# Optimization experiments

Hardware: AMD Instinct MI355X
Metric: run time of the kernel (lower is better)

Reference implementation:

```python
import jax, jax.numpy as jnp
import numpy as np

DIM = 1024
HID = 2048
OUT = 1024
NE = 8
TOPK = 2

def _xavier(key, shape):
    fan_in, fan_out = shape[-2], shape[-1]
    lim = jnp.sqrt(6.0 / (fan_in + fan_out))
    return jax.random.uniform(key, shape, jnp.float32, -lim, lim)

def setup_inputs() -> dict:
    key = jax.random.key(0)
    ks = jax.random.split(key, 8)
    X = jax.random.normal(ks[0], (4, 1024, DIM), jnp.float32)
    # stacked expert params: [NE, ...]
    W1 = _xavier(ks[1], (NE, DIM, HID))
    W3 = _xavier(ks[2], (NE, DIM, HID))
    W2 = _xavier(ks[3], (NE, HID, OUT))
    b1 = jnp.zeros((NE, HID), jnp.float32)
    b3 = jnp.zeros((NE, HID), jnp.float32)
    b2 = jnp.zeros((NE, OUT), jnp.float32)
    Wg = _xavier(ks[4], (DIM, NE))
    bg = jnp.zeros((NE,), jnp.float32)
    Wf = _xavier(ks[5], (OUT, OUT))
    bf = jnp.zeros((OUT,), jnp.float32)
    return {"X": X, "W1": W1, "b1": b1, "W3": W3, "b3": b3, "W2": W2, "b2": b2,
            "Wg": Wg, "bg": bg, "Wf": Wf, "bf": bf}

def reference(X, W1, b1, W3, b3, W2, b2, Wg, bg, Wf, bf):
    # gating: [B,S,E]
    gating = jax.nn.softmax(X @ Wg + bg, axis=-1)
    # top-k via argsort (matches original: ascending sort, take last k)
    top_k_indices = jnp.argsort(gating, axis=-1)[..., -TOPK:]  # [B,S,K]
    # dense all-expert SwiGLU FFN: [B,S,E,O]
    h1 = jnp.einsum('bsd,edh->bseh', X, W1) + b1  # [B,S,E,H]
    h3 = jnp.einsum('bsd,edh->bseh', X, W3) + b3
    h = jax.nn.silu(h1 * h3)
    expert_outputs = jnp.einsum('bseh,eho->bseo', h, W2) + b2  # [B,S,E,O]
    # gather top-k expert outputs
    topk_out = jnp.take_along_axis(expert_outputs, top_k_indices[..., None], axis=2)  # [B,S,K,O]
    topk_w = jnp.take_along_axis(gating, top_k_indices, axis=-1)  # [B,S,K]
    mixed = jnp.sum(topk_w[..., None] * topk_out, axis=2)  # [B,S,O]
    return mixed @ Wf + bf
```

## Files before the change

kernel.cpp:

```cpp
#include <hip/hip_runtime.h>

#define DIM  1024
#define HID  2048
#define OUTD 1024
#define NE   8
#define NTOK 4096

using bf16x8 = __attribute__((ext_vector_type(8))) short;
using f32x4  = __attribute__((ext_vector_type(4))) float;

__device__ __forceinline__ unsigned short f2bf(float f) {
  unsigned int u = __builtin_bit_cast(unsigned int, f);
  u += 0x7fff + ((u >> 16) & 1);
  return (unsigned short)(u >> 16);
}
__device__ __forceinline__ float b2f(unsigned short u) {
  unsigned int v = (unsigned int)u << 16;
  return __builtin_bit_cast(float, v);
}

__device__ __forceinline__ void gload16(const void* g, void* l) {
  __builtin_amdgcn_global_load_lds(
      (const __attribute__((address_space(1))) void*)g,
      (__attribute__((address_space(3))) void*)l, 16, 0, 0);
}

__device__ __forceinline__ void tc_tile(const float* __restrict__ inp, int C,
                                        unsigned short* __restrict__ op, int R,
                                        int c0, int r0, float (*tile)[33],
                                        int interleave, int s) {
  int tx = threadIdx.x & 31, ty = threadIdx.x >> 5;
#pragma unroll
  for (int j = 0; j < 4; j++)
    tile[ty + j * 8][tx] = inp[(size_t)(r0 + ty + j * 8) * C + c0 + tx];
  __syncthreads();
  int c = threadIdx.x >> 3, q = threadIdx.x & 7;
  int h = c0 + c;
  int orow = interleave ? (32 * (h >> 4) + 16 * s + (h & 15)) : h;
  ushort4 u;
  u.x = f2bf(tile[q * 4 + 0][c]); u.y = f2bf(tile[q * 4 + 1][c]);
  u.z = f2bf(tile[q * 4 + 2][c]); u.w = f2bf(tile[q * 4 + 3][c]);
  *(ushort4*)&op[(size_t)orow * R + r0 + q * 4] = u;
}

__global__ void tcast_i_kernel(const float* __restrict__ W1,
                               const float* __restrict__ W3,
                               unsigned short* __restrict__ out) {
  __shared__ float tile[32][33];
  int z = blockIdx.z, e = z & 7, s = z >> 3;
  const float* inp = (s ? W3 : W1) + (size_t)e * DIM * HID;
  unsigned short* op = out + (size_t)e * 2 * HID * DIM;
  tc_tile(inp, HID, op, DIM, blockIdx.x * 32, blockIdx.y * 32, tile, 1, s);
}

__global__ void tcast2_kernel(const float* __restrict__ W2, const float* __restrict__ Wf,
                              unsigned short* __restrict__ W2t,
                              unsigned short* __restrict__ Wft) {
  __shared__ float tile[32][33];
  int z = blockIdx.z;
  if (z < NE) {
    tc_tile(W2 + (size_t)z * HID * OUTD, OUTD, W2t + (size_t)z * OUTD * HID, HID,
            blockIdx.x * 32, blockIdx.y * 32, tile, 0, 0);
  } else {
    if (blockIdx.y >= DIM / 32) return;
    tc_tile(Wf, OUTD, Wft, DIM, blockIdx.x * 32, blockIdx.y * 32, tile, 0, 0);
  }
}

__global__ __launch_bounds__(256) void gating_kernel(
    const float* __restrict__ X, const float* __restrict__ Wg,
    const float* __restrict__ bg, unsigned short* __restrict__ Xb,
    int* __restrict__ topk_pack, float* __restrict__ topk_w,
    int* __restrict__ blkcnt) {
  __shared__ float wgs[NE][DIM];
  __shared__ int hist[NE];
  const int tid = threadIdx.x;
  for (int d = tid; d < DIM; d += 256) {
#pragma unroll
    for (int e = 0; e < NE; e++) wgs[e][d] = Wg[d * NE + e];
  }
  if (tid < NE) hist[tid] = 0;
  __syncthreads();
  const int wave = tid >> 6, lane = tid & 63;
  for (int tk = wave; tk < 32; tk += 4) {
    const int t = blockIdx.x * 32 + tk;
    const float* xr = X + (size_t)t * DIM;
    {
      const float4* xp = (const float4*)(xr + lane * 16);
      float4 v0 = xp[0], v1 = xp[1], v2 = xp[2], v3 = xp[3];
      uint4 w0, w1;
      w0.x = f2bf(v0.x) | ((unsigned)f2bf(v0.y) << 16);
      w0.y = f2bf(v0.z) | ((unsigned)f2bf(v0.w) << 16);
      w0.z = f2bf(v1.x) | ((unsigned)f2bf(v1.y) << 16);
      w0.w = f2bf(v1.z) | ((unsigned)f2bf(v1.w) << 16);
      w1.x = f2bf(v2.x) | ((unsigned)f2bf(v2.y) << 16);
      w1.y = f2bf(v2.z) | ((unsigned)f2bf(v2.w) << 16);
      w1.z = f2bf(v3.x) | ((unsigned)f2bf(v3.y) << 16);
      w1.w = f2bf(v3.z) | ((unsigned)f2bf(v3.w) << 16);
      uint4* op2 = (uint4*)(Xb + (size_t)t * DIM + lane * 16);
      op2[0] = w0; op2[1] = w1;
    }
    float acc[NE];
#pragma unroll
    for (int e = 0; e < NE; e++) acc[e] = 0.f;
#pragma unroll
    for (int j = 0; j < 16; j++) {
      float xv = xr[lane + j * 64];
#pragma unroll
      for (int e = 0; e < NE; e++) acc[e] += xv * wgs[e][lane + j * 64];
    }
#pragma unroll
    for (int e = 0; e < NE; e++) {
#pragma unroll
      for (int off = 32; off > 0; off >>= 1) acc[e] += __shfl_xor(acc[e], off, 64);
    }
    if (lane == 0) {
      float p[NE];
      float mx = -1e30f;
#pragma unroll
      for (int e = 0; e < NE; e++) { p[e] = acc[e] + bg[e]; mx = fmaxf(mx, p[e]); }
      float sum = 0.f;
#pragma unroll
      for (int e = 0; e < NE; e++) { p[e] = expf(p[e] - mx); sum += p[e]; }
      float inv = 1.f / sum;
#pragma unroll
      for (int e = 0; e < NE; e++) p[e] *= inv;
      int i1 = 0; float v1 = p[0];
#pragma unroll
      for (int e = 1; e < NE; e++) if (p[e] >= v1) { v1 = p[e]; i1 = e; }
      int i2 = (i1 == 0) ? 1 : 0; float v2 = p[i2];
#pragma unroll
      for (int e = 0; e < NE; e++) {
        if (e == i1) continue;
        if (p[e] >= v2 && e != i2) { v2 = p[e]; i2 = e; }
      }
      topk_pack[t] = i1 | (i2 << 4);
      topk_w[t * 2 + 0] = v1; topk_w[t * 2 + 1] = v2;
      atomicAdd(&hist[i1], 1); atomicAdd(&hist[i2], 1);
    }
  }
  __syncthreads();
  if (tid < NE) blkcnt[blockIdx.x * NE + tid] = hist[tid];
}

__global__ void scatter_kernel(const int* __restrict__ blkcnt,
                               const int* __restrict__ topk_pack,
                               int* __restrict__ counts, int* __restrict__ row_start,
                               int* __restrict__ tp, int* __restrict__ list) {
  __shared__ int lofs[NE];
  const int lane = threadIdx.x;
  const int myb = blockIdx.x;
  int s = 0, t = 0;
#pragma unroll
  for (int e = 0; e < NE; e++) {
    int c0 = blkcnt[lane * NE + e], c1 = blkcnt[(lane + 64) * NE + e];
    int tote = c0 + c1;
    int pre = (lane < myb ? c0 : 0) + (lane + 64 < myb ? c1 : 0);
#pragma unroll
    for (int off = 32; off > 0; off >>= 1) {
      tote += __shfl_xor(tote, off, 64);
      pre  += __shfl_xor(pre,  off, 64);
    }
    if (lane == 0) lofs[e] = s + pre;
    if (myb == 0 && lane == 0) { counts[e] = tote; row_start[e] = s; tp[e] = t; }
    s += tote; t += (tote + 127) >> 7;
  }
  if (myb == 0 && lane == 0) tp[NE] = t;
  __syncthreads();
  if (lane < 32) {
    int tok = myb * 32 + lane;
    int pk = topk_pack[tok];
    int e1 = pk & 15, e2 = (pk >> 4) & 15;
    int p1 = atomicAdd(&lofs[e1], 1); list[p1] = tok << 1;
    int p2 = atomicAdd(&lofs[e2], 1); list[p2] = (tok << 1) | 1;
  }
}

__global__ __launch_bounds__(512, 4) void ffn_a_kernel(
    const unsigned short* __restrict__ Xb,
    const unsigned short* __restrict__ W13t,
    const float* __restrict__ b1, const float* __restrict__ b3,
    const int* __restrict__ counts, const int* __restrict__ row_start,
    const int* __restrict__ tp, const int* __restrict__ list,
    unsigned short* __restrict__ h_buf) {
  __shared__ unsigned short S[24576];
  const int by = blockIdx.y;
  if (by >= tp[NE]) return;
  int e = 0;
#pragma unroll
  for (int k = 1; k < NE; k++) if (by >= tp[k]) e = k;
  const int ne = counts[e], rs = row_start[e];
  const int m0 = (by - tp[e]) * 128;
  const int n0 = blockIdx.x * 256;

  const int tid = threadIdx.x;
  const int wave = tid >> 6, lane = tid & 63;
  const int lr = lane & 15, lk = lane >> 4;
  const int wm = (wave & 1) * 64, wn = (wave >> 1) * 64;

  const int scs = ((lane & 7) ^ (lane >> 3)) * 8;
  const unsigned short* asrc[2];
  const unsigned short* bsrc[4];
#pragma unroll
  for (int i = 0; i < 2; i++) {
    int sr = i * 64 + wave * 8 + (lane >> 3);
    int rr = m0 + sr; if (rr >= ne) rr = m0;
    int tok = list[rs + rr] >> 1;
    asrc[i] = Xb + (size_t)tok * DIM + scs;
  }
#pragma unroll
  for (int c = 0; c < 4; c++) {
    int sr = c * 64 + wave * 8 + (lane >> 3);
    bsrc[c] = W13t + ((size_t)e * 2 * HID + n0 + sr) * DIM + scs;
  }

  f32x4 acc[4][4];
  const f32x4 zero = {0.f, 0.f, 0.f, 0.f};
#pragma unroll
  for (int m = 0; m < 4; m++)
#pragma unroll
    for (int n = 0; n < 4; n++) acc[m][n] = zero;

  const int sx = lr & 7;

  for (int k0 = 0; k0 < DIM; k0 += 64) {
#pragma unroll
    for (int i = 0; i < 2; i++)
      gload16(asrc[i] + k0, &S[(i * 64 + wave * 8) * 64]);
#pragma unroll
    for (int c = 0; c < 4; c++)
      gload16(bsrc[c] + k0, &S[8192 + (c * 64 + wave * 8) * 64]);
    __syncthreads();
#pragma unroll
    for (int kk = 0; kk < 2; kk++) {
      const int sl = ((kk * 4 + lk) ^ sx) * 8;
      bf16x8 a[4], b[4];
#pragma unroll
      for (int m = 0; m < 4; m++)
        a[m] = *(const bf16x8*)&S[(wm + m * 16 + lr) * 64 + sl];
#pragma unroll
      for (int n = 0; n < 4; n++)
        b[n] = *(const bf16x8*)&S[8192 + (wn + n * 16 + lr) * 64 + sl];
#pragma unroll
      for (int m = 0; m < 4; m++)
#pragma unroll
        for (int n = 0; n < 4; n++)
          acc[m][n] = __builtin_amdgcn_mfma_f32_16x16x32_bf16(a[m], b[n], acc[m][n], 0, 0, 0);
    }
    __syncthreads();
  }

  const int hq = (n0 + wn) >> 5;
#pragma unroll
  for (int g = 0; g < 2; g++) {
    int h = (hq + g) * 16 + lr;
    float b1v = b1[e * HID + h];
    float b3v = b3[e * HID + h];
#pragma unroll
    for (int m = 0; m < 4; m++) {
#pragma unroll
      for (int j = 0; j < 4; j++) {
        int rr = m0 + wm + m * 16 + lk * 4 + j;
        if (rr < ne) {
          float h1 = acc[m][2 * g][j] + b1v;
          float h3 = acc[m][2 * g + 1][j] + b3v;
          float v = h1 * h3;
          h_buf[(size_t)(rs + rr) * HID + h] = f2bf(v / (1.f + expf(-v)));
        }
      }
    }
  }
}

__global__ __launch_bounds__(256, 3) void ffn_b_kernel(
    const unsigned short* __restrict__ h_buf,
    const unsigned short* __restrict__ W2t,
    const float* __restrict__ b2,
    const int* __restrict__ counts, const int* __restrict__ row_start,
    const int* __restrict__ tp, const int* __restrict__ list,
    const float* __restrict__ topk_w, unsigned short* __restrict__ ob) {
  __shared__ unsigned short As[128 * 64];
  __shared__ unsigned short Bs[128 * 64];
  const int by = blockIdx.y;
  if (by >= tp[NE]) return;
  int e = 0;
#pragma unroll
  for (int k = 1; k < NE; k++) if (by >= tp[k]) e = k;
  const int ne = counts[e], rs = row_start[e];
  const int m0 = (by - tp[e]) * 128;
  const int n0 = blockIdx.x * 128;

  const int tid = threadIdx.x;
  const int wave = tid >> 6, lane = tid & 63;
  const int lr = lane & 15, lk = lane >> 4;
  const int wm = (wave >> 1) * 64, wn = (wave & 1) * 64;

  const int scs = ((lane & 7) ^ (lane >> 3)) * 8;
  const unsigned short* asrc[4];
  const unsigned short* bsrc[4];
#pragma unroll
  for (int i = 0; i < 4; i++) {
    int sr = (wave * 4 + i) * 8 + (lane >> 3);
    asrc[i] = h_buf + (size_t)(rs + m0 + sr) * HID + scs;
    bsrc[i] = W2t + ((size_t)e * OUTD + n0 + sr) * HID + scs;
  }

  f32x4 acc[4][4];
  const f32x4 zero = {0.f, 0.f, 0.f, 0.f};
#pragma unroll
  for (int m = 0; m < 4; m++)
#pragma unroll
    for (int n = 0; n < 4; n++) acc[m][n] = zero;

  const int sx = lr & 7;

  for (int k0 = 0; k0 < HID; k0 += 64) {
#pragma unroll
    for (int i = 0; i < 4; i++) {
      gload16(asrc[i] + k0, &As[(wave * 4 + i) * 512]);
      gload16(bsrc[i] + k0, &Bs[(wave * 4 + i) * 512]);
    }
    __syncthreads();
#pragma unroll
    for (int kk = 0; kk < 2; kk++) {
      const int sl = ((kk * 4 + lk) ^ sx) * 8;
      bf16x8 a[4], b[4];
#pragma unroll
      for (int m = 0; m < 4; m++)
        a[m] = *(const bf16x8*)&As[(wm + m * 16 + lr) * 64 + sl];
#pragma unroll
      for (int n = 0; n < 4; n++)
        b[n] = *(const bf16x8*)&Bs[(wn + n * 16 + lr) * 64 + sl];
#pragma unroll
      for (int m = 0; m < 4; m++)
#pragma unroll
        for (int n = 0; n < 4; n++)
          acc[m][n] = __builtin_amdgcn_mfma_f32_16x16x32_bf16(a[m], b[n], acc[m][n], 0, 0, 0);
    }
    __syncthreads();
  }

#pragma unroll
  for (int n = 0; n < 4; n++) {
    int col = n0 + wn + n * 16 + lr;
    float b2v = b2[e * OUTD + col];
#pragma unroll
    for (int m = 0; m < 4; m++) {
#pragma unroll
      for (int j = 0; j < 4; j++) {
        int rr = m0 + wm + m * 16 + lk * 4 + j;
        if (rr < ne) {
          int entry = list[rs + rr];
          float w = topk_w[entry];
          ob[(size_t)entry * OUTD + col] = f2bf(w * (acc[m][n][j] + b2v));
        }
      }
    }
  }
}

__global__ __launch_bounds__(256) void final_kernel(
    const unsigned short* __restrict__ ob, const unsigned short* __restrict__ Wft,
    const float* __restrict__ bfv, float* __restrict__ out) {
  const int bid = blockIdx.x;
  const int n0 = (bid >> 5) * 128;
  const int m0 = ((bid & 7) + 8 * ((bid >> 3) & 3)) * 128;

  __shared__ unsigned short As[128 * 64];
  __shared__ unsigned short Bs[128 * 64];

  const int tid = threadIdx.x;
  const int wave = tid >> 6, lane = tid & 63;
  const int lrow = lane >> 3;
  const int lcol = (lane & 7) * 8;

  const unsigned short* bsrc[4];
#pragma unroll
  for (int i = 0; i < 4; i++) {
    int sr = (wave * 4 + i) * 8 + lrow;
    bsrc[i] = Wft + (size_t)(n0 + sr) * DIM + lcol;
  }

  const int wm = (wave >> 1) * 64, wn = (wave & 1) * 64;
  const int lr = lane & 15, lk = lane >> 4;

  f32x4 acc[4][4];
  const f32x4 zero = {0.f, 0.f, 0.f, 0.f};
#pragma unroll
  for (int m = 0; m < 4; m++)
#pragma unroll
    for (int n = 0; n < 4; n++) acc[m][n] = zero;

  for (int k0 = 0; k0 < DIM; k0 += 64) {
#pragma unroll
    for (int g = 0; g < 8; g++) {
      int idx = g * 256 + tid;
      int r = idx >> 4;
      int c4 = (idx & 15) * 4;
      ushort4 a0 = *(const ushort4*)&ob[((size_t)(m0 + r) * 2) * OUTD + k0 + c4];
      ushort4 a1 = *(const ushort4*)&ob[((size_t)(m0 + r) * 2 + 1) * OUTD + k0 + c4];
      ushort4 u;
      u.x = f2bf(b2f(a0.x) + b2f(a1.x)); u.y = f2bf(b2f(a0.y) + b2f(a1.y));
      u.z = f2bf(b2f(a0.z) + b2f(a1.z)); u.w = f2bf(b2f(a0.w) + b2f(a1.w));
      *(ushort4*)&As[r * 64 + c4] = u;
    }
#pragma unroll
    for (int i = 0; i < 4; i++) gload16(bsrc[i] + k0, &Bs[(wave * 4 + i) * 512]);
    __syncthreads();
#pragma unroll
    for (int kk = 0; kk < 2; kk++) {
      bf16x8 a[4], b[4];
#pragma unroll
      for (int m = 0; m < 4; m++)
        a[m] = *(const bf16x8*)&As[(wm + m * 16 + lr) * 64 + kk * 32 + lk * 8];
#pragma unroll
      for (int n = 0; n < 4; n++)
        b[n] = *(const bf16x8*)&Bs[(wn + n * 16 + lr) * 64 + kk * 32 + lk * 8];
#pragma unroll
      for (int m = 0; m < 4; m++)
#pragma unroll
        for (int n = 0; n < 4; n++)
          acc[m][n] = __builtin_amdgcn_mfma_f32_16x16x32_bf16(a[m], b[n], acc[m][n], 0, 0, 0);
    }
    __syncthreads();
  }

#pragma unroll
  for (int n = 0; n < 4; n++) {
    int col = n0 + wn + n * 16 + lr;
    float bv = bfv[col];
#pragma unroll
    for (int m = 0; m < 4; m++) {
#pragma unroll
      for (int j = 0; j < 4; j++) {
        int r = m0 + wm + m * 16 + lk * 4 + j;
        out[(size_t)r * OUTD + col] = acc[m][n][j] + bv;
      }
    }
  }
}

extern "C" void kernel_launch(void* const* d_in, const int* in_sizes, int n_in,
                              void* d_out, int out_size, void* d_ws, size_t ws_size,
                              hipStream_t stream) {
  const float* X   = (const float*)d_in[0];
  const float* W1  = (const float*)d_in[1];
  const float* b1  = (const float*)d_in[2];
  const float* W3  = (const float*)d_in[3];
  const float* b3  = (const float*)d_in[4];
  const float* W2  = (const float*)d_in[5];
  const float* b2  = (const float*)d_in[6];
  const float* Wg  = (const float*)d_in[7];
  const float* bg  = (const float*)d_in[8];
  const float* Wf  = (const float*)d_in[9];
  const float* bfv = (const float*)d_in[10];
  float* out = (float*)d_out;

  char* p = (char*)d_ws;
  auto alloc = [&](size_t bytes) { char* r = p; p += (bytes + 255) & ~(size_t)255; return r; };
  unsigned short* Xb   = (unsigned short*)alloc((size_t)NTOK * DIM * 2);
  unsigned short* W13t = (unsigned short*)alloc((size_t)NE * 2 * HID * DIM * 2);
  unsigned short* W2t  = (unsigned short*)alloc((size_t)NE * OUTD * HID * 2);
  unsigned short* Wft  = (unsigned short*)alloc((size_t)OUTD * DIM * 2);
  unsigned short* hbuf = (unsigned short*)alloc((size_t)(NTOK * 2 + 256) * HID * 2);
  unsigned short* ob   = (unsigned short*)alloc((size_t)NTOK * 2 * OUTD * 2);
  int* topk_pack       = (int*)alloc(NTOK * 4);
  float* topk_w        = (float*)alloc(NTOK * 2 * 4);
  int* counts          = (int*)alloc(NE * 4);
  int* row_start       = (int*)alloc(NE * 4);
  int* tp              = (int*)alloc((NE + 1) * 4);
  int* blkcnt          = (int*)alloc(128 * NE * 4);
  int* list            = (int*)alloc(NTOK * 2 * 4);

  gating_kernel<<<128, 256, 0, stream>>>(X, Wg, bg, Xb, topk_pack, topk_w, blkcnt);
  tcast_i_kernel<<<dim3(HID / 32, DIM / 32, 16), 256, 0, stream>>>(W1, W3, W13t);
  tcast2_kernel<<<dim3(OUTD / 32, HID / 32, NE + 1), 256, 0, stream>>>(W2, Wf, W2t, Wft);

  scatter_kernel<<<128, 64, 0, stream>>>(blkcnt, topk_pack, counts, row_start, tp, list);

  ffn_a_kernel<<<dim3(2 * HID / 256, 72), 512, 0, stream>>>(
      Xb, W13t, b1, b3, counts, row_start, tp, list, hbuf);
  ffn_b_kernel<<<dim3(OUTD / 128, 72), 256, 0, stream>>>(
      hbuf, W2t, b2, counts, row_start, tp, list, topk_w, ob);
  final_kernel<<<256, 256, 0, stream>>>(ob, Wft, bfv, out);
}
```

Baseline: 315.8 us.

## Shrink GEMM K-tile to 32 with 128x128 blocks and merge weight-cast kernels

The two weight transpose/cast kernels become one flat-grid launch, removing a kernel boundary. Both expert GEMM kernels now use 256-thread blocks with 128x128 output tiles and a 32-wide K step, using half the LDS per block and a new swizzle, with launch bounds raised to 6 blocks per CU. The aim is higher occupancy so more blocks can hide latency. In exchange there are twice as many barriers per unit of K, and ffn_a has half the tile width, so operand reuse per block is lower.

```diff
diff --git a/kernel.cpp b/kernel.cpp
--- a/kernel.cpp
+++ b/kernel.cpp
@@ -43,27 +43,27 @@
   *(ushort4*)&op[(size_t)orow * R + r0 + q * 4] = u;
 }
 
-__global__ void tcast_i_kernel(const float* __restrict__ W1,
-                               const float* __restrict__ W3,
-                               unsigned short* __restrict__ out) {
+__global__ void tcast_all_kernel(const float* __restrict__ W1, const float* __restrict__ W3,
+                                 const float* __restrict__ W2, const float* __restrict__ Wf,
+                                 unsigned short* __restrict__ W13t,
+                                 unsigned short* __restrict__ W2t,
+                                 unsigned short* __restrict__ Wft) {
   __shared__ float tile[32][33];
-  int z = blockIdx.z, e = z & 7, s = z >> 3;
-  const float* inp = (s ? W3 : W1) + (size_t)e * DIM * HID;
-  unsigned short* op = out + (size_t)e * 2 * HID * DIM;
-  tc_tile(inp, HID, op, DIM, blockIdx.x * 32, blockIdx.y * 32, tile, 1, s);
-}
-
-__global__ void tcast2_kernel(const float* __restrict__ W2, const float* __restrict__ Wf,
-                              unsigned short* __restrict__ W2t,
-                              unsigned short* __restrict__ Wft) {
-  __shared__ float tile[32][33];
-  int z = blockIdx.z;
-  if (z < NE) {
+  int b = blockIdx.x;
+  if (b < 32768) {
+    int z = b >> 11, rem = b & 2047;
+    int e = z & 7, s = z >> 3;
+    tc_tile((s ? W3 : W1) + (size_t)e * DIM * HID, HID,
+            W13t + (size_t)e * 2 * HID * DIM, DIM,
+            (rem & 63) * 32, (rem >> 6) * 32, tile, 1, s);
+  } else if (b < 49152) {
+    int i = b - 32768;
+    int z = i >> 11, rem = i & 2047;
     tc_tile(W2 + (size_t)z * HID * OUTD, OUTD, W2t + (size_t)z * OUTD * HID, HID,
-            blockIdx.x * 32, blockIdx.y * 32, tile, 0, 0);
+            (rem & 31) * 32, (rem >> 5) * 32, tile, 0, 0);
   } else {
-    if (blockIdx.y >= DIM / 32) return;
-    tc_tile(Wf, OUTD, Wft, DIM, blockIdx.x * 32, blockIdx.y * 32, tile, 0, 0);
+    int i = b - 49152;
+    tc_tile(Wf, OUTD, Wft, DIM, (i & 31) * 32, (i >> 5) * 32, tile, 0, 0);
   }
 }
 
@@ -176,14 +176,15 @@
   }
 }
 
-__global__ __launch_bounds__(512, 4) void ffn_a_kernel(
+__global__ __launch_bounds__(256, 6) void ffn_a_kernel(
     const unsigned short* __restrict__ Xb,
     const unsigned short* __restrict__ W13t,
     const float* __restrict__ b1, const float* __restrict__ b3,
     const int* __restrict__ counts, const int* __restrict__ row_start,
     const int* __restrict__ tp, const int* __restrict__ list,
     unsigned short* __restrict__ h_buf) {
-  __shared__ unsigned short S[24576];
+  __shared__ unsigned short As[128 * 32];
+  __shared__ unsigned short Bs[128 * 32];
   const int by = blockIdx.y;
   if (by >= tp[NE]) return;
   int e = 0;
@@ -191,27 +192,23 @@
   for (int k = 1; k < NE; k++) if (by >= tp[k]) e = k;
   const int ne = counts[e], rs = row_start[e];
   const int m0 = (by - tp[e]) * 128;
-  const int n0 = blockIdx.x * 256;
+  const int n0 = blockIdx.x * 128;
 
   const int tid = threadIdx.x;
   const int wave = tid >> 6, lane = tid & 63;
   const int lr = lane & 15, lk = lane >> 4;
-  const int wm = (wave & 1) * 64, wn = (wave >> 1) * 64;
-
-  const int scs = ((lane & 7) ^ (lane >> 3)) * 8;
+  const int wm = (wave >> 1) * 64, wn = (wave & 1) * 64;
+
+  const int scs = ((lane & 3) ^ ((lane >> 3) & 3)) * 8;
   const unsigned short* asrc[2];
-  const unsigned short* bsrc[4];
+  const unsigned short* bsrc[2];
 #pragma unroll
   for (int i = 0; i < 2; i++) {
-    int sr = i * 64 + wave * 8 + (lane >> 3);
+    int sr = (wave * 2 + i) * 16 + (lane >> 2);
     int rr = m0 + sr; if (rr >= ne) rr = m0;
     int tok = list[rs + rr] >> 1;
     asrc[i] = Xb + (size_t)tok * DIM + scs;
-  }
-#pragma unroll
-  for (int c = 0; c < 4; c++) {
-    int sr = c * 64 + wave * 8 + (lane >> 3);
-    bsrc[c] = W13t + ((size_t)e * 2 * HID + n0 + sr) * DIM + scs;
+    bsrc[i] = W13t + ((size_t)e * 2 * HID + n0 + sr) * DIM + scs;
   }
 
   f32x4 acc[4][4];
@@ -221,32 +218,27 @@
 #pragma unroll
     for (int n = 0; n < 4; n++) acc[m][n] = zero;
 
-  const int sx = lr & 7;
-
-  for (int k0 = 0; k0 < DIM; k0 += 64) {
-#pragma unroll
-    for (int i = 0; i < 2; i++)
-      gload16(asrc[i] + k0, &S[(i * 64 + wave * 8) * 64]);
-#pragma unroll
-    for (int c = 0; c < 4; c++)
-      gload16(bsrc[c] + k0, &S[8192 + (c * 64 + wave * 8) * 64]);
-    __syncthreads();
-#pragma unroll
-    for (int kk = 0; kk < 2; kk++) {
-      const int sl = ((kk * 4 + lk) ^ sx) * 8;
-      bf16x8 a[4], b[4];
-#pragma unroll
-      for (int m = 0; m < 4; m++)
-        a[m] = *(const bf16x8*)&S[(wm + m * 16 + lr) * 64 + sl];
+  const int sl = (lk ^ ((lr >> 1) & 3)) * 8;
+
+  for (int k0 = 0; k0 < DIM; k0 += 32) {
+#pragma unroll
+    for (int i = 0; i < 2; i++) {
+      gload16(asrc[i] + k0, &As[(wave * 2 + i) * 512]);
+      gload16(bsrc[i] + k0, &Bs[(wave * 2 + i) * 512]);
+    }
+    __syncthreads();
+    bf16x8 a[4], b[4];
+#pragma unroll
+    for (int m = 0; m < 4; m++)
+      a[m] = *(const bf16x8*)&As[(wm + m * 16 + lr) * 32 + sl];
+#pragma unroll
+    for (int n = 0; n < 4; n++)
+      b[n] = *(const bf16x8*)&Bs[(wn + n * 16 + lr) * 32 + sl];
+#pragma unroll
+    for (int m = 0; m < 4; m++)
 #pragma unroll
       for (int n = 0; n < 4; n++)
-        b[n] = *(const bf16x8*)&S[8192 + (wn + n * 16 + lr) * 64 + sl];
-#pragma unroll
-      for (int m = 0; m < 4; m++)
-#pragma unroll
-        for (int n = 0; n < 4; n++)
-          acc[m][n] = __builtin_amdgcn_mfma_f32_16x16x32_bf16(a[m], b[n], acc[m][n], 0, 0, 0);
-    }
+        acc[m][n] = __builtin_amdgcn_mfma_f32_16x16x32_bf16(a[m], b[n], acc[m][n], 0, 0, 0);
     __syncthreads();
   }
 
@@ -272,15 +264,15 @@
   }
 }
 
-__global__ __launch_bounds__(256, 3) void ffn_b_kernel(
+__global__ __launch_bounds__(256, 6) void ffn_b_kernel(
     const unsigned short* __restrict__ h_buf,
     const unsigned short* __restrict__ W2t,
     const float* __restrict__ b2,
     const int* __restrict__ counts, const int* __restrict__ row_start,
     const int* __restrict__ tp, const int* __restrict__ list,
     const float* __restrict__ topk_w, unsigned short* __restrict__ ob) {
-  __shared__ unsigned short As[128 * 64];
-  __shared__ unsigned short Bs[128 * 64];
+  __shared__ unsigned short As[128 * 32];
+  __shared__ unsigned short Bs[128 * 32];
   const int by = blockIdx.y;
   if (by >= tp[NE]) return;
   int e = 0;
@@ -295,12 +287,12 @@
   const int lr = lane & 15, lk = lane >> 4;
   const int wm = (wave >> 1) * 64, wn = (wave & 1) * 64;
 
-  const int scs = ((lane & 7) ^ (lane >> 3)) * 8;
-  const unsigned short* asrc[4];
-  const unsigned short* bsrc[4];
-#pragma unroll
-  for (int i = 0; i < 4; i++) {
-    int sr = (wave * 4 + i) * 8 + (lane >> 3);
+  const int scs = ((lane & 3) ^ ((lane >> 3) & 3)) * 8;
+  const unsigned short* asrc[2];
+  const unsigned short* bsrc[2];
+#pragma unroll
+  for (int i = 0; i < 2; i++) {
+    int sr = (wave * 2 + i) * 16 + (lane >> 2);
     asrc[i] = h_buf + (size_t)(rs + m0 + sr) * HID + scs;
     bsrc[i] = W2t + ((size_t)e * OUTD + n0 + sr) * HID + scs;
   }
@@ -312,31 +304,27 @@
 #pragma unroll
     for (int n = 0; n < 4; n++) acc[m][n] = zero;
 
-  const int sx = lr & 7;
-
-  for (int k0 = 0; k0 < HID; k0 += 64) {
-#pragma unroll
-    for (int i = 0; i < 4; i++) {
-      gload16(asrc[i] + k0, &As[(wave * 4 + i) * 512]);
-      gload16(bsrc[i] + k0, &Bs[(wave * 4 + i) * 512]);
-    }
-    __syncthreads();
-#pragma unroll
-    for (int kk = 0; kk < 2; kk++) {
-      const int sl = ((kk * 4 + lk) ^ sx) * 8;
-      bf16x8 a[4], b[4];
-#pragma unroll
-      for (int m = 0; m < 4; m++)
-        a[m] = *(const bf16x8*)&As[(wm + m * 16 + lr) * 64 + sl];
+  const int sl = (lk ^ ((lr >> 1) & 3)) * 8;
+
+  for (int k0 = 0; k0 < HID; k0 += 32) {
+#pragma unroll
+    for (int i = 0; i < 2; i++) {
+      gload16(asrc[i] + k0, &As[(wave * 2 + i) * 512]);
+      gload16(bsrc[i] + k0, &Bs[(wave * 2 + i) * 512]);
+    }
+    __syncthreads();
+    bf16x8 a[4], b[4];
+#pragma unroll
+    for (int m = 0; m < 4; m++)
+      a[m] = *(const bf16x8*)&As[(wm + m * 16 + lr) * 32 + sl];
+#pragma unroll
+    for (int n = 0; n < 4; n++)
+      b[n] = *(const bf16x8*)&Bs[(wn + n * 16 + lr) * 32 + sl];
+#pragma unroll
+    for (int m = 0; m < 4; m++)
 #pragma unroll
       for (int n = 0; n < 4; n++)
-        b[n] = *(const bf16x8*)&Bs[(wn + n * 16 + lr) * 64 + sl];
-#pragma unroll
-      for (int m = 0; m < 4; m++)
-#pragma unroll
-        for (int n = 0; n < 4; n++)
-          acc[m][n] = __builtin_amdgcn_mfma_f32_16x16x32_bf16(a[m], b[n], acc[m][n], 0, 0, 0);
-    }
+        acc[m][n] = __builtin_amdgcn_mfma_f32_16x16x32_bf16(a[m], b[n], acc[m][n], 0, 0, 0);
     __syncthreads();
   }
 
@@ -473,12 +461,11 @@
   int* list            = (int*)alloc(NTOK * 2 * 4);
 
   gating_kernel<<<128, 256, 0, stream>>>(X, Wg, bg, Xb, topk_pack, topk_w, blkcnt);
-  tcast_i_kernel<<<dim3(HID / 32, DIM / 32, 16), 256, 0, stream>>>(W1, W3, W13t);
-  tcast2_kernel<<<dim3(OUTD / 32, HID / 32, NE + 1), 256, 0, stream>>>(W2, Wf, W2t, Wft);
+  tcast_all_kernel<<<50176, 256, 0, stream>>>(W1, W3, W2, Wf, W13t, W2t, Wft);
 
   scatter_kernel<<<128, 64, 0, stream>>>(blkcnt, topk_pack, counts, row_start, tp, list);
 
-  ffn_a_kernel<<<dim3(2 * HID / 256, 72), 512, 0, stream>>>(
+  ffn_a_kernel<<<dim3(2 * HID / 128, 72), 256, 0, stream>>>(
       Xb, W13t, b1, b3, counts, row_start, tp, list, hbuf);
   ffn_b_kernel<<<dim3(OUTD / 128, 72), 256, 0, stream>>>(
       hbuf, W2t, b2, counts, row_start, tp, list, topk_w, ob);
```

Result: slower. 1.014 ms (+220.9%).
